# Optimization experiments

Measured on AMD Instinct MI355X. Metric: run time of the kernel, lower is better.

## Reference

```python
import jax, jax.numpy as jnp
import numpy as np

B = 4096          # batch
IN = 4096         # in_features
OUT = 4096        # out_features
MASK_DENSITY = 0.1

def setup_inputs() -> dict:
    key = jax.random.key(0)
    k1, k2, k3, k4, k5 = jax.random.split(key, 5)
    x = jax.random.normal(k1, (B, IN), dtype=jnp.float32)
    # truncated-normal-ish init, std 0.1 (plain normal scaled is fine for a numeric baseline)
    weight = jax.random.normal(k2, (OUT, IN), dtype=jnp.float32) * 0.1
    bound = 1.0 / np.sqrt(IN)
    bias = jax.random.uniform(k3, (OUT,), dtype=jnp.float32, minval=-bound, maxval=bound)
    mask = jax.random.bernoulli(k4, MASK_DENSITY, (OUT, IN))  # bool, fixed sparsity pattern
    residual_connection = jax.random.randint(k5, (OUT,), 0, IN, dtype=jnp.int32)
    return {"x": x, "weight": weight, "bias": bias, "mask": mask,
            "residual_connection": residual_connection}

def reference(x, weight, bias, mask, residual_connection):
    # out = relu(x @ (mask * W)^T + b) + x[:, residual_connection]
    w_masked = jnp.where(mask, weight, 0.0)              # [OUT, IN]
    out = x @ w_masked.T + bias                          # [B, OUT]
    out = jax.nn.relu(out)
    out = jnp.take(x, residual_connection, axis=1) + out # gathered residual add
    return out
```

## Files before the change

kernel.cpp:

```cpp
#include <hip/hip_runtime.h>
#include <hip/hip_bf16.h>
#include <stdint.h>

#define B_ROWS 4096
#define IN_F   4096
#define OUT_F  4096

#define BM 256
#define BN 256
#define BK 64
#define NKT (IN_F / BK)

typedef float  f32x4  __attribute__((ext_vector_type(4)));
typedef short  bf16x8 __attribute__((ext_vector_type(8)));
typedef unsigned short u16x4 __attribute__((ext_vector_type(4)));

#define AS1 __attribute__((address_space(1)))
#define AS3 __attribute__((address_space(3)))

__device__ __forceinline__ uint16_t f2bf_rne(float f) {
    uint32_t u = __float_as_uint(f);
    uint32_t r = u + 0x7fffu + ((u >> 16) & 1u);
    return (uint16_t)(r >> 16);
}
__device__ __forceinline__ float bf2f(uint16_t h) {
    return __uint_as_float(((uint32_t)h) << 16);
}

__global__ __launch_bounds__(256) void cvt_x_t_kernel(
    const float* __restrict__ x, uint16_t* __restrict__ xb, uint16_t* __restrict__ xbT)
{
    __shared__ float t[64][65];
    const int r0 = blockIdx.y * 64;
    const int c0 = blockIdx.x * 64;
    const int tid = threadIdx.x;
    const int lr = tid >> 4;
    const int lc4 = (tid & 15) * 4;

#pragma unroll
    for (int p = 0; p < 4; ++p) {
        const int row = p * 16 + lr;
        float4 v = *(const float4*)(x + (size_t)(r0 + row) * IN_F + c0 + lc4);
        ushort4 o;
        o.x = f2bf_rne(v.x); o.y = f2bf_rne(v.y);
        o.z = f2bf_rne(v.z); o.w = f2bf_rne(v.w);
        *(ushort4*)(xb + (size_t)(r0 + row) * IN_F + c0 + lc4) = o;
        t[row][lc4 + 0] = v.x; t[row][lc4 + 1] = v.y;
        t[row][lc4 + 2] = v.z; t[row][lc4 + 3] = v.w;
    }
    __syncthreads();
#pragma unroll
    for (int p = 0; p < 4; ++p) {
        const int c = p * 16 + lr;
        ushort4 o;
        o.x = f2bf_rne(t[lc4 + 0][c]);
        o.y = f2bf_rne(t[lc4 + 1][c]);
        o.z = f2bf_rne(t[lc4 + 2][c]);
        o.w = f2bf_rne(t[lc4 + 3][c]);
        *(ushort4*)(xbT + (size_t)(c0 + c) * B_ROWS + r0 + lc4) = o;
    }
}

__global__ void detect_mask_kernel(const uint32_t* __restrict__ mraw, int* __restrict__ flag) {
    __shared__ uint32_t red[256];
    uint32_t acc = 0;
    for (int k = threadIdx.x; k < 1024; k += 256) acc |= mraw[k];
    red[threadIdx.x] = acc;
    __syncthreads();
    for (int s = 128; s > 0; s >>= 1) {
        if (threadIdx.x < s) red[threadIdx.x] |= red[threadIdx.x + s];
        __syncthreads();
    }
    if (threadIdx.x == 0) *flag = (red[0] & 0xFFFFFF00u) ? 1 : 0;
}

__global__ void cvt_w_kernel(const float* __restrict__ w, const void* __restrict__ mraw,
                             const int* __restrict__ flag, uint16_t* __restrict__ wb) {
    int i = (blockIdx.x * 256 + threadIdx.x) * 4;
    float4 v = *(const float4*)(w + i);
    int m0, m1, m2, m3;
    if (*flag) {
        uchar4 mm = *(const uchar4*)((const uint8_t*)mraw + i);
        m0 = mm.x; m1 = mm.y; m2 = mm.z; m3 = mm.w;
    } else {
        int4 mm = *(const int4*)((const int*)mraw + i);
        m0 = mm.x; m1 = mm.y; m2 = mm.z; m3 = mm.w;
    }
    ushort4 o;
    o.x = m0 ? f2bf_rne(v.x) : (uint16_t)0;
    o.y = m1 ? f2bf_rne(v.y) : (uint16_t)0;
    o.z = m2 ? f2bf_rne(v.z) : (uint16_t)0;
    o.w = m3 ? f2bf_rne(v.w) : (uint16_t)0;
    *(ushort4*)(wb + i) = o;
}

__global__ __launch_bounds__(512, 2) void gemm_kernel(
    const uint16_t* __restrict__ xb, const uint16_t* __restrict__ wb,
    const uint16_t* __restrict__ xbT, const float* __restrict__ bias,
    const int* __restrict__ rc, float* __restrict__ out)
{
    __shared__ alignas(16) uint16_t Abuf[2][2][128 * BK];
    __shared__ alignas(16) uint16_t Bbuf[2][2][128 * BK];
    __shared__ float bias_s[BN];
    __shared__ int   rc_s[BN];

    const int tid = threadIdx.x;

    const int bid = blockIdx.x;
    const int wg  = (bid & 7) * 32 + (bid >> 3);
    const int row0 = (wg >> 4) * BM;
    const int col0 = (wg & 15) * BN;

    const int wave = tid >> 6, lane = tid & 63;
    const int wm = wave >> 1;
    const int wn = wave & 1;
    const int quad = lane >> 4, l16 = lane & 15;
    const int swr = (l16 & 7) << 3;

    const int srow = tid >> 3;
    const int ssw  = ((tid & 7) ^ (srow & 7)) << 3;
    const uint16_t* pA0 = xb + (size_t)(row0 + srow) * IN_F + ssw;
    const uint16_t* pB0 = wb + (size_t)(col0 + srow) * IN_F + ssw;
    const uint16_t* pA1 = pA0 + (size_t)128 * IN_F;
    const uint16_t* pB1 = pB0 + (size_t)128 * IN_F;

    auto stage = [&](const uint16_t* src, uint16_t* ldsdst, size_t ko) {
        __builtin_amdgcn_global_load_lds((const AS1 void*)(src + ko),
                                         (AS3 void*)(ldsdst + tid * 8), 16, 0, 0);
        __builtin_amdgcn_global_load_lds((const AS1 void*)(src + ko + (size_t)64 * IN_F),
                                         (AS3 void*)(ldsdst + tid * 8 + 4096), 16, 0, 0);
    };

    if (tid < BN) {
        __builtin_amdgcn_global_load_lds((const AS1 void*)(bias + col0 + tid),
                                         (AS3 void*)(bias_s + tid), 4, 0, 0);
        __builtin_amdgcn_global_load_lds((const AS1 void*)(rc + col0 + tid),
                                         (AS3 void*)(rc_s + tid), 4, 0, 0);
    }

    f32x4 acc[4][2][4];
#pragma unroll
    for (int q = 0; q < 4; ++q)
#pragma unroll
        for (int mi = 0; mi < 2; ++mi)
#pragma unroll
            for (int ni = 0; ni < 4; ++ni)
                acc[q][mi][ni] = (f32x4){0.f, 0.f, 0.f, 0.f};

    stage(pA0, &Abuf[0][0][0], 0);
    stage(pB0, &Bbuf[0][0][0], 0);
    stage(pA1, &Abuf[0][1][0], 0);
    stage(pB1, &Bbuf[0][1][0], 0);

    bf16x8 a[2][2];
    bf16x8 b[4][2];

#define WAIT_VM4() asm volatile("s_waitcnt vmcnt(4)" ::: "memory")
#define BARRIER()  do { __builtin_amdgcn_s_barrier(); asm volatile("" ::: "memory"); } while (0)

    for (int t = 0; t < NKT; ++t) {
        const int cur = t & 1, nxt = cur ^ 1;
        const size_t koff = (size_t)(t + 1) * BK;

        auto load_a = [&](int mh) {
#pragma unroll
            for (int mi = 0; mi < 2; ++mi) {
                const int rA = wm * 32 + mi * 16 + l16;
#pragma unroll
                for (int ks = 0; ks < 2; ++ks)
                    a[mi][ks] = *(const bf16x8*)__builtin_assume_aligned(
                        (const void*)(&Abuf[cur][mh][rA * BK + ((ks * 32 + (quad << 3)) ^ swr)]), 16);
            }
        };
        auto load_b = [&](int nh) {
#pragma unroll
            for (int ni = 0; ni < 4; ++ni) {
                const int rB = wn * 64 + ni * 16 + l16;
#pragma unroll
                for (int ks = 0; ks < 2; ++ks)
                    b[ni][ks] = *(const bf16x8*)__builtin_assume_aligned(
                        (const void*)(&Bbuf[cur][nh][rB * BK + ((ks * 32 + (quad << 3)) ^ swr)]), 16);
            }
        };
        auto mfma_q = [&](int q) {
            __builtin_amdgcn_s_setprio(1);
#pragma unroll
            for (int mi = 0; mi < 2; ++mi)
#pragma unroll
                for (int ni = 0; ni < 4; ++ni) {
                    acc[q][mi][ni] = __builtin_amdgcn_mfma_f32_16x16x32_bf16(
                        a[mi][0], b[ni][0], acc[q][mi][ni], 0, 0, 0);
                    acc[q][mi][ni] = __builtin_amdgcn_mfma_f32_16x16x32_bf16(
                        a[mi][1], b[ni][1], acc[q][mi][ni], 0, 0, 0);
                }
            __builtin_amdgcn_s_setprio(0);
        };

        WAIT_VM4();
        BARRIER();
        load_a(0); load_b(0);
        stage(pA0, &Abuf[nxt][0][0], koff);
        mfma_q(0);

        WAIT_VM4();
        BARRIER();
        load_a(1);
        stage(pB0, &Bbuf[nxt][0][0], koff);
        mfma_q(1);

        WAIT_VM4();
        BARRIER();
        load_b(1);
        stage(pA1, &Abuf[nxt][1][0], koff);
        mfma_q(2);

        BARRIER();
        load_a(0);
        stage(pB1, &Bbuf[nxt][1][0], koff);
        mfma_q(3);
    }

#undef WAIT_VM4
#undef BARRIER

    const int QMH[4] = {0, 1, 1, 0};
    const int QNH[4] = {0, 0, 1, 1};
#pragma unroll
    for (int q = 0; q < 4; ++q) {
        const int mh = QMH[q], nh = QNH[q];
#pragma unroll
        for (int ni = 0; ni < 4; ++ni) {
            const int lcol = nh * 128 + wn * 64 + ni * 16 + l16;
            const int gcol = col0 + lcol;
            const float bv = bias_s[lcol];
            const int   rv = rc_s[lcol];
#pragma unroll
            for (int mi = 0; mi < 2; ++mi) {
                const int grow0 = row0 + mh * 128 + wm * 32 + mi * 16 + quad * 4;
                u16x4 xq = *(const u16x4*)(xbT + (size_t)rv * B_ROWS + grow0);
#pragma unroll
                for (int r = 0; r < 4; ++r) {
                    float v = fmaxf(acc[q][mi][ni][r] + bv, 0.0f) + bf2f(xq[r]);
                    out[(size_t)(grow0 + r) * OUT_F + gcol] = v;
                }
            }
        }
    }
}

extern "C" void kernel_launch(void* const* d_in, const int* in_sizes, int n_in,
                              void* d_out, int out_size, void* d_ws, size_t ws_size,
                              hipStream_t stream) {
    const float* x    = (const float*)d_in[0];
    const float* w    = (const float*)d_in[1];
    const float* bias = (const float*)d_in[2];
    const void*  mask = (const void*)d_in[3];
    const int*   rc   = (const int*)d_in[4];
    float* out = (float*)d_out;

    uint16_t* xb   = (uint16_t*)d_ws;
    uint16_t* wb   = xb  + (size_t)B_ROWS * IN_F;
    uint16_t* xbT  = wb  + (size_t)OUT_F * IN_F;
    int*      flag = (int*)(xbT + (size_t)IN_F * B_ROWS);

    detect_mask_kernel<<<1, 256, 0, stream>>>((const uint32_t*)mask, flag);
    {
        dim3 g(IN_F / 64, B_ROWS / 64);
        cvt_x_t_kernel<<<g, 256, 0, stream>>>(x, xb, xbT);
    }
    cvt_w_kernel<<<(OUT_F * IN_F) / (256 * 4), 256, 0, stream>>>(w, mask, flag, wb);

    gemm_kernel<<<dim3((B_ROWS / BM) * (OUT_F / BN)), dim3(512), 0, stream>>>(
        xb, wb, xbT, bias, rc, out);
}
```

Measured before the change: 360.8 us.

## Rework GEMM wave tiling to 2x4 waves with inline-asm LDS reads

```diff
diff --git a/kernel.cpp b/kernel.cpp
--- a/kernel.cpp
+++ b/kernel.cpp
@@ -17,6 +17,8 @@
 
 #define AS1 __attribute__((address_space(1)))
 #define AS3 __attribute__((address_space(3)))
+
+template<int N> struct IC { static constexpr int v = N; };
 
 __device__ __forceinline__ uint16_t f2bf_rne(float f) {
     uint32_t u = __float_as_uint(f);
@@ -94,6 +96,13 @@
     *(ushort4*)(wb + i) = o;
 }
 
+__device__ __forceinline__ bf16x8 ds_read128(uint32_t off) {
+    bf16x8 r;
+    asm volatile("ds_read_b128 %0, %1" : "=v"(r) : "v"(off));
+    return r;
+}
+#define LDSOFF(p) ((uint32_t)(uintptr_t)(AS3 void*)(p))
+
 __global__ __launch_bounds__(512, 2) void gemm_kernel(
     const uint16_t* __restrict__ xb, const uint16_t* __restrict__ wb,
     const uint16_t* __restrict__ xbT, const float* __restrict__ bias,
@@ -112,10 +121,18 @@
     const int col0 = (wg & 15) * BN;
 
     const int wave = tid >> 6, lane = tid & 63;
-    const int wm = wave >> 1;
-    const int wn = wave & 1;
+    const int wm = wave >> 2;
+    const int wn = wave & 3;
+    const int bh = wn >> 1;
     const int quad = lane >> 4, l16 = lane & 15;
     const int swr = (l16 & 7) << 3;
+    const int e0  = (quad << 3) ^ swr;
+    const uint32_t kd = (uint32_t)(((e0 ^ 32) - e0) * 2);
+
+    const uint32_t aOff0 = LDSOFF(&Abuf[0][wm][0]) + (uint32_t)((l16 * BK + e0) * 2);
+    const uint32_t aOff1 = LDSOFF(&Abuf[1][wm][0]) + (uint32_t)((l16 * BK + e0) * 2);
+    const uint32_t bOff0 = LDSOFF(&Bbuf[0][bh][0]) + (uint32_t)((((wn & 1) * 64 + l16) * BK + e0) * 2);
+    const uint32_t bOff1 = LDSOFF(&Bbuf[1][bh][0]) + (uint32_t)((((wn & 1) * 64 + l16) * BK + e0) * 2);
 
     const int srow = tid >> 3;
     const int ssw  = ((tid & 7) ^ (srow & 7)) << 3;
@@ -138,111 +155,134 @@
                                          (AS3 void*)(rc_s + tid), 4, 0, 0);
     }
 
-    f32x4 acc[4][2][4];
-#pragma unroll
-    for (int q = 0; q < 4; ++q)
-#pragma unroll
-        for (int mi = 0; mi < 2; ++mi)
-#pragma unroll
-            for (int ni = 0; ni < 4; ++ni)
-                acc[q][mi][ni] = (f32x4){0.f, 0.f, 0.f, 0.f};
+    f32x4 acc[8][4];
+#pragma unroll
+    for (int mi = 0; mi < 8; ++mi)
+#pragma unroll
+        for (int ni = 0; ni < 4; ++ni)
+            acc[mi][ni] = (f32x4){0.f, 0.f, 0.f, 0.f};
 
     stage(pA0, &Abuf[0][0][0], 0);
+    stage(pA1, &Abuf[0][1][0], 0);
     stage(pB0, &Bbuf[0][0][0], 0);
-    stage(pA1, &Abuf[0][1][0], 0);
     stage(pB1, &Bbuf[0][1][0], 0);
 
-    bf16x8 a[2][2];
-    bf16x8 b[4][2];
-
-#define WAIT_VM4() asm volatile("s_waitcnt vmcnt(4)" ::: "memory")
-#define BARRIER()  do { __builtin_amdgcn_s_barrier(); asm volatile("" ::: "memory"); } while (0)
-
-    for (int t = 0; t < NKT; ++t) {
-        const int cur = t & 1, nxt = cur ^ 1;
+#define LGKM0() do { asm volatile("s_waitcnt lgkmcnt(0)" ::: "memory"); \
+                     __builtin_amdgcn_sched_barrier(0); } while (0)
+
+    auto tile = [&](auto curc, int t) {
+        constexpr int CUR = decltype(curc)::v;
+        constexpr int NXT = CUR ^ 1;
+        const uint32_t aB = CUR ? aOff1 : aOff0;
+        const uint32_t bB = CUR ? bOff1 : bOff0;
         const size_t koff = (size_t)(t + 1) * BK;
 
-        auto load_a = [&](int mh) {
-#pragma unroll
-            for (int mi = 0; mi < 2; ++mi) {
-                const int rA = wm * 32 + mi * 16 + l16;
-#pragma unroll
-                for (int ks = 0; ks < 2; ++ks)
-                    a[mi][ks] = *(const bf16x8*)__builtin_assume_aligned(
-                        (const void*)(&Abuf[cur][mh][rA * BK + ((ks * 32 + (quad << 3)) ^ swr)]), 16);
-            }
-        };
-        auto load_b = [&](int nh) {
+        bf16x8 a[2][2], b[4][2];
+
+        asm volatile("s_waitcnt vmcnt(0)" ::: "memory");
+        __builtin_amdgcn_s_barrier();
+
+#pragma unroll
+        for (int ni = 0; ni < 4; ++ni) {
+            b[ni][0] = ds_read128(bB + ni * 2048);
+            b[ni][1] = ds_read128(bB + ni * 2048 + kd);
+        }
+#pragma unroll
+        for (int m2 = 0; m2 < 2; ++m2) {
+            a[m2][0] = ds_read128(aB + m2 * 2048);
+            a[m2][1] = ds_read128(aB + m2 * 2048 + kd);
+        }
+        stage(pA0, &Abuf[NXT][0][0], koff);
+        stage(pA1, &Abuf[NXT][1][0], koff);
+        __builtin_amdgcn_s_barrier();
+        LGKM0();
+        __builtin_amdgcn_s_setprio(1);
+#pragma unroll
+        for (int m2 = 0; m2 < 2; ++m2)
 #pragma unroll
             for (int ni = 0; ni < 4; ++ni) {
-                const int rB = wn * 64 + ni * 16 + l16;
-#pragma unroll
-                for (int ks = 0; ks < 2; ++ks)
-                    b[ni][ks] = *(const bf16x8*)__builtin_assume_aligned(
-                        (const void*)(&Bbuf[cur][nh][rB * BK + ((ks * 32 + (quad << 3)) ^ swr)]), 16);
-            }
-        };
-        auto mfma_q = [&](int q) {
-            __builtin_amdgcn_s_setprio(1);
-#pragma unroll
-            for (int mi = 0; mi < 2; ++mi)
-#pragma unroll
-                for (int ni = 0; ni < 4; ++ni) {
-                    acc[q][mi][ni] = __builtin_amdgcn_mfma_f32_16x16x32_bf16(
-                        a[mi][0], b[ni][0], acc[q][mi][ni], 0, 0, 0);
-                    acc[q][mi][ni] = __builtin_amdgcn_mfma_f32_16x16x32_bf16(
-                        a[mi][1], b[ni][1], acc[q][mi][ni], 0, 0, 0);
-                }
-            __builtin_amdgcn_s_setprio(0);
-        };
-
-        WAIT_VM4();
-        BARRIER();
-        load_a(0); load_b(0);
-        stage(pA0, &Abuf[nxt][0][0], koff);
-        mfma_q(0);
-
-        WAIT_VM4();
-        BARRIER();
-        load_a(1);
-        stage(pB0, &Bbuf[nxt][0][0], koff);
-        mfma_q(1);
-
-        WAIT_VM4();
-        BARRIER();
-        load_b(1);
-        stage(pA1, &Abuf[nxt][1][0], koff);
-        mfma_q(2);
-
-        BARRIER();
-        load_a(0);
-        stage(pB1, &Bbuf[nxt][1][0], koff);
-        mfma_q(3);
-    }
-
-#undef WAIT_VM4
-#undef BARRIER
-
-    const int QMH[4] = {0, 1, 1, 0};
-    const int QNH[4] = {0, 0, 1, 1};
-#pragma unroll
-    for (int q = 0; q < 4; ++q) {
-        const int mh = QMH[q], nh = QNH[q];
-#pragma unroll
-        for (int ni = 0; ni < 4; ++ni) {
-            const int lcol = nh * 128 + wn * 64 + ni * 16 + l16;
-            const int gcol = col0 + lcol;
-            const float bv = bias_s[lcol];
-            const int   rv = rc_s[lcol];
-#pragma unroll
-            for (int mi = 0; mi < 2; ++mi) {
-                const int grow0 = row0 + mh * 128 + wm * 32 + mi * 16 + quad * 4;
-                u16x4 xq = *(const u16x4*)(xbT + (size_t)rv * B_ROWS + grow0);
-#pragma unroll
-                for (int r = 0; r < 4; ++r) {
-                    float v = fmaxf(acc[q][mi][ni][r] + bv, 0.0f) + bf2f(xq[r]);
-                    out[(size_t)(grow0 + r) * OUT_F + gcol] = v;
-                }
+                acc[m2][ni] = __builtin_amdgcn_mfma_f32_16x16x32_bf16(a[m2][0], b[ni][0], acc[m2][ni], 0, 0, 0);
+                acc[m2][ni] = __builtin_amdgcn_mfma_f32_16x16x32_bf16(a[m2][1], b[ni][1], acc[m2][ni], 0, 0, 0);
+            }
+        __builtin_amdgcn_s_setprio(0);
+        __builtin_amdgcn_s_barrier();
+
+#pragma unroll
+        for (int m2 = 0; m2 < 2; ++m2) {
+            a[m2][0] = ds_read128(aB + (2 + m2) * 2048);
+            a[m2][1] = ds_read128(aB + (2 + m2) * 2048 + kd);
+        }
+        stage(pB0, &Bbuf[NXT][0][0], koff);
+        stage(pB1, &Bbuf[NXT][1][0], koff);
+        __builtin_amdgcn_s_barrier();
+        LGKM0();
+        __builtin_amdgcn_s_setprio(1);
+#pragma unroll
+        for (int m2 = 0; m2 < 2; ++m2)
+#pragma unroll
+            for (int ni = 0; ni < 4; ++ni) {
+                acc[2 + m2][ni] = __builtin_amdgcn_mfma_f32_16x16x32_bf16(a[m2][0], b[ni][0], acc[2 + m2][ni], 0, 0, 0);
+                acc[2 + m2][ni] = __builtin_amdgcn_mfma_f32_16x16x32_bf16(a[m2][1], b[ni][1], acc[2 + m2][ni], 0, 0, 0);
+            }
+        __builtin_amdgcn_s_setprio(0);
+        __builtin_amdgcn_s_barrier();
+
+#pragma unroll
+        for (int m2 = 0; m2 < 2; ++m2) {
+            a[m2][0] = ds_read128(aB + (4 + m2) * 2048);
+            a[m2][1] = ds_read128(aB + (4 + m2) * 2048 + kd);
+        }
+        __builtin_amdgcn_s_barrier();
+        LGKM0();
+        __builtin_amdgcn_s_setprio(1);
+#pragma unroll
+        for (int m2 = 0; m2 < 2; ++m2)
+#pragma unroll
+            for (int ni = 0; ni < 4; ++ni) {
+                acc[4 + m2][ni] = __builtin_amdgcn_mfma_f32_16x16x32_bf16(a[m2][0], b[ni][0], acc[4 + m2][ni], 0, 0, 0);
+                acc[4 + m2][ni] = __builtin_amdgcn_mfma_f32_16x16x32_bf16(a[m2][1], b[ni][1], acc[4 + m2][ni], 0, 0, 0);
+            }
+        __builtin_amdgcn_s_setprio(0);
+        __builtin_amdgcn_s_barrier();
+
+#pragma unroll
+        for (int m2 = 0; m2 < 2; ++m2) {
+            a[m2][0] = ds_read128(aB + (6 + m2) * 2048);
+            a[m2][1] = ds_read128(aB + (6 + m2) * 2048 + kd);
+        }
+        __builtin_amdgcn_s_barrier();
+        LGKM0();
+        __builtin_amdgcn_s_setprio(1);
+#pragma unroll
+        for (int m2 = 0; m2 < 2; ++m2)
+#pragma unroll
+            for (int ni = 0; ni < 4; ++ni) {
+                acc[6 + m2][ni] = __builtin_amdgcn_mfma_f32_16x16x32_bf16(a[m2][0], b[ni][0], acc[6 + m2][ni], 0, 0, 0);
+                acc[6 + m2][ni] = __builtin_amdgcn_mfma_f32_16x16x32_bf16(a[m2][1], b[ni][1], acc[6 + m2][ni], 0, 0, 0);
+            }
+        __builtin_amdgcn_s_setprio(0);
+    };
+
+    for (int tt = 0; tt < NKT; tt += 2) {
+        tile(IC<0>{}, tt);
+        tile(IC<1>{}, tt + 1);
+    }
+#undef LGKM0
+
+#pragma unroll
+    for (int ni = 0; ni < 4; ++ni) {
+        const int lcol = wn * 64 + ni * 16 + l16;
+        const int gcol = col0 + lcol;
+        const float bv = bias_s[lcol];
+        const int   rv = rc_s[lcol];
+#pragma unroll
+        for (int mi = 0; mi < 8; ++mi) {
+            const int grow0 = row0 + wm * 128 + mi * 16 + quad * 4;
+            u16x4 xq = *(const u16x4*)(xbT + (size_t)rv * B_ROWS + grow0);
+#pragma unroll
+            for (int r = 0; r < 4; ++r) {
+                float v = fmaxf(acc[mi][ni][r] + bv, 0.0f) + bf2f(xq[r]);
+                out[(size_t)(grow0 + r) * OUT_F + gcol] = v;
             }
         }
     }
```

Measured after the change: 350.9 us. 1.03x faster.
